# Kernel tuning notes

Hardware: AMD Instinct MI355X
Metric: run time of the kernel (lower is better)

## Reference

```python
import jax, jax.numpy as jnp
import numpy as np
import math

D_MODEL = 256
N_LEVELS = 4
N_HEADS = 8
N_POINTS = 4
N_FRAME = 4
SHAPES = [(80, 80), (40, 40), (20, 20), (10, 10)]  # sum H*W = 8500
NB = 2
T1 = 4
T2 = 4
LEN_Q = 8500


def _grid_init_bias():
    # replicate torch _reset_parameters grid bias for sampling_offsets
    thetas = np.arange(N_HEADS, dtype=np.float32) * (2.0 * math.pi / N_HEADS)
    grid = np.stack([np.cos(thetas), np.sin(thetas)], -1)
    grid = grid / np.abs(grid).max(-1, keepdims=True)
    grid = np.tile(grid[:, None, None, :], (1, N_LEVELS, N_POINTS, 1))
    grid = grid * (np.arange(N_POINTS, dtype=np.float32) + 1.0)[None, None, :, None]
    return jnp.asarray(grid.reshape(-1), jnp.float32)


def setup_inputs() -> dict:
    key = jax.random.key(0)
    ks = jax.random.split(key, 8)
    Len_in = sum(h * w for h, w in SHAPES)
    query = jax.random.normal(ks[0], (NB, T1, LEN_Q, D_MODEL), jnp.float32)
    reference_points = jax.random.uniform(ks[1], (NB, T1, LEN_Q, N_LEVELS, 2), jnp.float32)
    input_flatten = jax.random.normal(ks[2], (NB, T2, Len_in, D_MODEL), jnp.float32)
    input_spatial_shapes = jnp.array(SHAPES, jnp.int32)
    starts = np.cumsum([0] + [h * w for h, w in SHAPES])[:-1]
    input_level_start_index = jnp.asarray(starts, jnp.int32)
    s = 0.01
    W_off = jax.random.normal(ks[3], (D_MODEL, N_HEADS * N_LEVELS * N_POINTS * 2), jnp.float32) * s
    b_off = _grid_init_bias()
    W_att = jax.random.normal(ks[4], (D_MODEL, N_HEADS * N_LEVELS * N_POINTS), jnp.float32) * s
    b_att = jnp.zeros((N_HEADS * N_LEVELS * N_POINTS,), jnp.float32)
    xav = 1.0 / math.sqrt(D_MODEL)
    W_val = jax.random.normal(ks[5], (D_MODEL, D_MODEL), jnp.float32) * xav
    b_val = jnp.zeros((D_MODEL,), jnp.float32)
    W_out = jax.random.normal(ks[6], (D_MODEL, D_MODEL), jnp.float32) * xav
    b_out = jnp.zeros((D_MODEL,), jnp.float32)
    return dict(query=query, reference_points=reference_points, input_flatten=input_flatten,
                input_spatial_shapes=input_spatial_shapes, input_level_start_index=input_level_start_index,
                W_off=W_off, b_off=b_off, W_att=W_att, b_att=b_att,
                W_val=W_val, b_val=b_val, W_out=W_out, b_out=b_out)


def _bilinear(v_flat, H, W, gx, gy):
    # v_flat: (B, d, H*W); gx,gy: (B, S) in [-1,1]; zeros padding, align_corners=False
    x = (gx + 1.0) * (W * 0.5) - 0.5
    y = (gy + 1.0) * (H * 0.5) - 0.5
    x0 = jnp.floor(x); y0 = jnp.floor(y)
    x1 = x0 + 1.0; y1 = y0 + 1.0
    wx1 = x - x0; wx0 = 1.0 - wx1
    wy1 = y - y0; wy0 = 1.0 - wy1

    def gather(xi, yi):
        valid = ((xi >= 0) & (xi < W) & (yi >= 0) & (yi < H)).astype(v_flat.dtype)
        xc = jnp.clip(xi, 0, W - 1).astype(jnp.int32)
        yc = jnp.clip(yi, 0, H - 1).astype(jnp.int32)
        idx = yc * W + xc  # (B, S)
        g = jnp.take_along_axis(v_flat, idx[:, None, :], axis=2)  # (B, d, S)
        return g * valid[:, None, :]

    return (gather(x0, y0) * (wx0 * wy0)[:, None, :]
            + gather(x1, y0) * (wx1 * wy0)[:, None, :]
            + gather(x0, y1) * (wx0 * wy1)[:, None, :]
            + gather(x1, y1) * (wx1 * wy1)[:, None, :])


def _core(value_t, locs, att, shapes):
    # value_t: (n, Len_in, M, d); locs: (n, Lq, M, L, P, 2); att: (n, Lq, M, L, P)
    n, Len_in, M, d = value_t.shape
    Lq, P = locs.shape[1], locs.shape[4]
    start = 0
    out = 0.0
    for l, (H, W) in enumerate(shapes):
        hw = H * W
        v = value_t[:, start:start + hw]  # (n, hw, M, d)
        start += hw
        v = v.transpose(0, 2, 3, 1).reshape(n * M, d, hw)
        g = locs[:, :, :, l] * 2.0 - 1.0  # (n, Lq, M, P, 2)
        g = g.transpose(0, 2, 1, 3, 4).reshape(n * M, Lq * P, 2)
        samp = _bilinear(v, H, W, g[..., 0], g[..., 1])  # (n*M, d, Lq*P)
        a = att[:, :, :, l].transpose(0, 2, 1, 3).reshape(n * M, 1, Lq * P)
        out = out + (samp * a).reshape(n, M, d, Lq, P).sum(-1)
    return out.transpose(0, 3, 1, 2).reshape(n, Lq, M * d)  # (n, Lq, C)


def reference(query, reference_points, input_flatten, input_spatial_shapes, input_level_start_index,
              W_off, b_off, W_att, b_att, W_val, b_val, W_out, b_out):
    shapes = [(int(h), int(w)) for h, w in np.asarray(input_spatial_shapes)]
    n, t1n, Lq, C = query.shape
    M, L, P = N_HEADS, N_LEVELS, N_POINTS
    d = C // M
    value = input_flatten @ W_val + b_val  # (n, T2, Len_in, C)
    value = value.reshape(n, value.shape[1], -1, M, d)
    normalizer = jnp.array([[w, h] for h, w in shapes], jnp.float32)  # (L, 2) = (W_l, H_l)
    outs = []
    for t1 in range(t1n):
        t2s = [t for t in (t1 - 1, t1, t1 + 1) if 0 <= t < N_FRAME]
        K = len(t2s)
        q = query[:, t1]  # (n, Lq, C)
        # all frames share ONE attention_weights Linear -> identical logits per t2
        logits = (q @ W_att + b_att).reshape(n, Lq, M, L, P)
        stacked = jnp.broadcast_to(logits[..., None], (n, Lq, M, L, P, K))
        att = jax.nn.softmax(stacked.reshape(n, Lq, M, L * P * K), axis=-1)
        att = att.reshape(n, Lq, M, L, P, K)
        # all frames share ONE sampling_offsets Linear -> identical locations per t2
        off = (q @ W_off + b_off).reshape(n, Lq, M, L, P, 2)
        off = off / normalizer[None, None, None, :, None, :]
        locs = reference_points[:, t1][:, :, None, :, None, :] + off  # (n,Lq,M,L,P,2)
        out_t1 = 0.0
        for k, t2 in enumerate(t2s):
            out_t1 = out_t1 + _core(value[:, t2], locs, att[..., k], shapes)
        outs.append(out_t1)
    out = jnp.stack(outs, axis=1)  # (n, T1, Lq, C)
    return out @ W_out + b_out
```

## Files before the change

kernel.cpp:

```cpp
#include <hip/hip_runtime.h>

#define LQ 8500

typedef _Float16 half8 __attribute__((ext_vector_type(8)));
typedef float f32x4 __attribute__((ext_vector_type(4)));

__device__ __forceinline__ unsigned short f2h(float f) {
    return __builtin_bit_cast(unsigned short, (_Float16)f);
}
__device__ __forceinline__ float hlo(unsigned w) {
    return (float)__builtin_bit_cast(_Float16, (unsigned short)(w & 0xffffu));
}
__device__ __forceinline__ float hhi(unsigned w) {
    return (float)__builtin_bit_cast(_Float16, (unsigned short)(w >> 16));
}
__device__ __forceinline__ unsigned pk2(float a, float b) {
    return (unsigned)f2h(a) | ((unsigned)f2h(b) << 16);
}

__global__ __launch_bounds__(256) void prep_weights(const float* __restrict__ Woff,
                                                    const float* __restrict__ boff,
                                                    const float* __restrict__ Watt,
                                                    const float* __restrict__ batt,
                                                    const float* __restrict__ Wval,
                                                    const float* __restrict__ Wout,
                                                    unsigned short* __restrict__ Wct,
                                                    unsigned short* __restrict__ Wvt,
                                                    unsigned short* __restrict__ Wot,
                                                    float* __restrict__ bcat) {
    int idx = blockIdx.x * 256 + threadIdx.x;
    if (idx < 98304) {
        int j = idx >> 8, k = idx & 255;
        float v = (j < 256) ? Woff[k * 256 + j] : Watt[k * 128 + (j - 256)];
        Wct[idx] = f2h(v);
    } else if (idx < 98304 + 65536) {
        int t = idx - 98304;
        int n = t >> 8, k = t & 255;
        Wvt[t] = f2h(Wval[k * 256 + n]);
    } else if (idx < 98304 + 131072) {
        int t = idx - 98304 - 65536;
        int n = t >> 8, k = t & 255;
        Wot[t] = f2h(Wout[k * 256 + n]);
    } else if (idx < 98304 + 131072 + 384) {
        int j = idx - 98304 - 131072;
        bcat[j] = (j < 256) ? boff[j] : batt[j - 256];
    }
}

template <int OUTMODE, int ASRC>
__global__ __launch_bounds__(256) void gemm_f16(const void* __restrict__ Avoid,
                                                const unsigned short* __restrict__ Bt,
                                                const float* __restrict__ bias,
                                                void* __restrict__ Cout, int M) {
    __shared__ char lds[32768];
    const int tid = threadIdx.x;
    const int r0 = blockIdx.x * 128, c0 = blockIdx.y * 128;
    const int wid = tid >> 6, lane = tid & 63;
    const int wr = (wid >> 1) * 64, wc = (wid & 1) * 64;

    f32x4 acc[4][4] = {};
    uint4 ra[2], rb[2];

#define LOADT(k0)                                                                      \
    {                                                                                  \
        _Pragma("unroll")                                                              \
        for (int cc = 0; cc < 2; ++cc) {                                               \
            int ch = cc * 256 + tid;                                                   \
            int row = ch >> 2, seg = ch & 3;                                           \
            uint4 va = {0, 0, 0, 0};                                                   \
            int ar = r0 + row;                                                         \
            if (ar < M) {                                                              \
                if (ASRC == 0) {                                                       \
                    va = *reinterpret_cast<const uint4*>(                              \
                        (const unsigned short*)Avoid + (size_t)ar * 256 + (k0) + seg * 8); \
                } else if (ASRC == 1) {                                                \
                    const float4* ap = reinterpret_cast<const float4*>(                \
                        (const float*)Avoid + (size_t)ar * 256 + (k0) + seg * 8);      \
                    float4 a = ap[0], b = ap[1];                                       \
                    va.x = pk2(a.x, a.y); va.y = pk2(a.z, a.w);                        \
                    va.z = pk2(b.x, b.y); va.w = pk2(b.z, b.w);                        \
                } else {                                                               \
                    int g = ar / LQ;                                                   \
                    int pos = ar - g * LQ;                                             \
                    int t1 = g & 3, n = g >> 2;                                        \
                    int t2a = t1 == 0 ? 0 : t1 - 1;                                    \
                    int t2b = t1 == 3 ? 3 : t1 + 1;                                    \
                    float4 s0 = {0, 0, 0, 0}, s1 = {0, 0, 0, 0};                       \
                    for (int t2 = t2a; t2 <= t2b; ++t2) {                              \
                        const float4* p = reinterpret_cast<const float4*>(             \
                            (const float*)Avoid +                                      \
                            ((size_t)(n * 4 + t2) * LQ + pos) * 256 + (k0) + seg * 8); \
                        float4 a = p[0], b = p[1];                                     \
                        s0.x += a.x; s0.y += a.y; s0.z += a.z; s0.w += a.w;            \
                        s1.x += b.x; s1.y += b.y; s1.z += b.z; s1.w += b.w;            \
                    }                                                                  \
                    va.x = pk2(s0.x, s0.y); va.y = pk2(s0.z, s0.w);                    \
                    va.z = pk2(s1.x, s1.y); va.w = pk2(s1.z, s1.w);                    \
                }                                                                      \
            }                                                                          \
            ra[cc] = va;                                                               \
            rb[cc] = *reinterpret_cast<const uint4*>(Bt + (size_t)(c0 + row) * 256 +   \
                                                     (k0) + seg * 8);                  \
        }                                                                              \
    }

#define STORET(b)                                                                      \
    {                                                                                  \
        _Pragma("unroll")                                                              \
        for (int cc = 0; cc < 2; ++cc) {                                               \
            int ch = cc * 256 + tid;                                                   \
            int row = ch >> 2, seg = ch & 3;                                           \
            int byte = (row << 6) + (seg << 4);                                        \
            int swz = byte ^ ((row & 7) << 4);                                         \
            *reinterpret_cast<uint4*>(lds + (b) * 16384 + swz) = ra[cc];               \
            *reinterpret_cast<uint4*>(lds + (b) * 16384 + 8192 + swz) = rb[cc];        \
        }                                                                              \
    }

    LOADT(0);
    STORET(0);
    __syncthreads();

    for (int t = 0; t < 8; ++t) {
        if (t < 7) LOADT((t + 1) * 32);
        char* base = lds + (t & 1) * 16384;
        half8 af[4], bf[4];
#pragma unroll
        for (int i = 0; i < 4; ++i) {
            int rowA = wr + i * 16 + (lane & 15);
            int byteA = (rowA << 6) + ((lane >> 4) << 4);
            af[i] = *reinterpret_cast<const half8*>(base + (byteA ^ ((rowA & 7) << 4)));
            int rowB = wc + i * 16 + (lane & 15);
            int byteB = (rowB << 6) + ((lane >> 4) << 4);
            bf[i] = *reinterpret_cast<const half8*>(base + 8192 + (byteB ^ ((rowB & 7) << 4)));
        }
#pragma unroll
        for (int i = 0; i < 4; ++i)
#pragma unroll
            for (int j = 0; j < 4; ++j)
                acc[i][j] = __builtin_amdgcn_mfma_f32_16x16x32_f16(af[i], bf[j], acc[i][j], 0, 0, 0);
        if (t < 7) STORET((t + 1) & 1);
        __syncthreads();
    }

#pragma unroll
    for (int j = 0; j < 4; ++j) {
        int col = c0 + wc + j * 16 + (lane & 15);
        float bv = bias[col];
#pragma unroll
        for (int i = 0; i < 4; ++i) {
#pragma unroll
            for (int r = 0; r < 4; ++r) {
                int row = r0 + wr + i * 16 + (lane >> 4) * 4 + r;
                if (row >= M) continue;
                float v = acc[i][j][r];
                if (OUTMODE == 1) {
                    int g = row / LQ;
                    int pos = row - g * LQ;
                    int t1 = g & 3;
                    float sc = (t1 == 0 || t1 == 3) ? 2.f : 3.f;
                    v += bv * sc;
                    int m = col >> 5, c = col & 31;
                    ((unsigned short*)Cout)[((size_t)(g * 8 + m) * LQ + pos) * 32 + c] = f2h(v);
                } else if (OUTMODE == 2) {
                    ((unsigned short*)Cout)[(size_t)row * 384 + col] = f2h(v + bv);
                } else {
                    ((float*)Cout)[(size_t)row * 256 + col] = v + bv;
                }
            }
        }
    }
#undef LOADT
#undef STORET
}

__global__ __launch_bounds__(256) void sample_kernel(const unsigned short* __restrict__ P,
                                                     const float* __restrict__ refp,
                                                     const unsigned short* __restrict__ Vs,
                                                     unsigned short* __restrict__ O16) {
    int tid = threadIdx.x, bid = blockIdx.x;
    int g = bid & 7;
    int q0 = (bid >> 3) * 16;
    int ql = tid >> 4, m = (tid >> 1) & 7, h = tid & 1;
    int q = q0 + ql;
    if (q >= LQ) return;

    const size_t qrow = (size_t)g * LQ + q;

    unsigned ow[16];
    {
        const uint4* po = reinterpret_cast<const uint4*>(P + qrow * 384 + m * 32);
        uint4 a = po[0], b = po[1], c = po[2], d = po[3];
        ow[0] = a.x; ow[1] = a.y; ow[2] = a.z; ow[3] = a.w;
        ow[4] = b.x; ow[5] = b.y; ow[6] = b.z; ow[7] = b.w;
        ow[8] = c.x; ow[9] = c.y; ow[10] = c.z; ow[11] = c.w;
        ow[12] = d.x; ow[13] = d.y; ow[14] = d.z; ow[15] = d.w;
    }
    float wgt[16];
    {
        const uint4* pa = reinterpret_cast<const uint4*>(P + qrow * 384 + 256 + m * 16);
        uint4 a = pa[0], b = pa[1];
        unsigned aw[8] = {a.x, a.y, a.z, a.w, b.x, b.y, b.z, b.w};
#pragma unroll
        for (int j = 0; j < 8; ++j) {
            wgt[j * 2 + 0] = hlo(aw[j]);
            wgt[j * 2 + 1] = hhi(aw[j]);
        }
        float mx = -1e30f;
#pragma unroll
        for (int j = 0; j < 16; ++j) mx = fmaxf(mx, wgt[j]);
        float s = 0.f;
#pragma unroll
        for (int j = 0; j < 16; ++j) { wgt[j] = __expf(wgt[j] - mx); s += wgt[j]; }
        int t1 = g & 3;
        float Kc = (t1 == 0 || t1 == 3) ? 2.f : 3.f;
        float inv = 1.f / (s * Kc);
#pragma unroll
        for (int j = 0; j < 16; ++j) wgt[j] *= inv;
    }

    float rx[4], ry[4];
    {
        const float4* rp = reinterpret_cast<const float4*>(refp + qrow * 8);
        float4 r0 = rp[0], r1 = rp[1];
        rx[0] = r0.x; ry[0] = r0.y; rx[1] = r0.z; ry[1] = r0.w;
        rx[2] = r1.x; ry[2] = r1.y; rx[3] = r1.z; ry[3] = r1.w;
    }

    float acc[16];
#pragma unroll
    for (int d = 0; d < 16; ++d) acc[d] = 0.f;

    const unsigned short* vplane = Vs + (size_t)(g * 8 + m) * (LQ * 32) + h * 16;

#pragma unroll 4
    for (int p = 0; p < 16; ++p) {
        const int l = p >> 2;
        const int Wl = 80 >> l;
        const int start = (l == 0) ? 0 : (l == 1) ? 6400 : (l == 2) ? 8000 : 8400;
        const float Wlf = (float)Wl;

        float x = fmaf(rx[l], Wlf, hlo(ow[p])) - 0.5f;
        float y = fmaf(ry[l], Wlf, hhi(ow[p])) - 0.5f;
        float w = wgt[p];

        float xf = floorf(x), yf = floorf(y);
        int x0 = (int)xf, y0 = (int)yf;
        float wx1 = x - xf, wy1 = y - yf;

        int xb = min(max(x0, 0), Wl - 2);
        float wl = (x0 == xb) ? 1.f - wx1 : ((x0 + 1 == xb) ? wx1 : 0.f);
        float wr = (x0 == xb) ? wx1 : ((x0 - 1 == xb) ? 1.f - wx1 : 0.f);

        int yc0 = min(max(y0, 0), Wl - 1);
        float cw0 = (y0 >= 0 && y0 < Wl) ? (1.f - wy1) * w : 0.f;
        int y1i = y0 + 1;
        int yc1 = min(max(y1i, 0), Wl - 1);
        float cw1 = (y1i >= 0 && y1i < Wl) ? wy1 * w : 0.f;

        const uint4* p0 = reinterpret_cast<const uint4*>(
            vplane + (size_t)(start + yc0 * Wl + xb) * 32);
        const uint4* p1 = reinterpret_cast<const uint4*>(
            vplane + (size_t)(start + yc1 * Wl + xb) * 32);
        uint4 L0a = p0[0], L0b = p0[1], R0a = p0[4], R0b = p0[5];
        uint4 L1a = p1[0], L1b = p1[1], R1a = p1[4], R1b = p1[5];

        float c0l = cw0 * wl, c0r = cw0 * wr;
        float c1l = cw1 * wl, c1r = cw1 * wr;

        acc[0]  += c0l * hlo(L0a.x) + c0r * hlo(R0a.x) + c1l * hlo(L1a.x) + c1r * hlo(R1a.x);
        acc[1]  += c0l * hhi(L0a.x) + c0r * hhi(R0a.x) + c1l * hhi(L1a.x) + c1r * hhi(R1a.x);
        acc[2]  += c0l * hlo(L0a.y) + c0r * hlo(R0a.y) + c1l * hlo(L1a.y) + c1r * hlo(R1a.y);
        acc[3]  += c0l * hhi(L0a.y) + c0r * hhi(R0a.y) + c1l * hhi(L1a.y) + c1r * hhi(R1a.y);
        acc[4]  += c0l * hlo(L0a.z) + c0r * hlo(R0a.z) + c1l * hlo(L1a.z) + c1r * hlo(R1a.z);
        acc[5]  += c0l * hhi(L0a.z) + c0r * hhi(R0a.z) + c1l * hhi(L1a.z) + c1r * hhi(R1a.z);
        acc[6]  += c0l * hlo(L0a.w) + c0r * hlo(R0a.w) + c1l * hlo(L1a.w) + c1r * hlo(R1a.w);
        acc[7]  += c0l * hhi(L0a.w) + c0r * hhi(R0a.w) + c1l * hhi(L1a.w) + c1r * hhi(R1a.w);
        acc[8]  += c0l * hlo(L0b.x) + c0r * hlo(R0b.x) + c1l * hlo(L1b.x) + c1r * hlo(R1b.x);
        acc[9]  += c0l * hhi(L0b.x) + c0r * hhi(R0b.x) + c1l * hhi(L1b.x) + c1r * hhi(R1b.x);
        acc[10] += c0l * hlo(L0b.y) + c0r * hlo(R0b.y) + c1l * hlo(L1b.y) + c1r * hlo(R1b.y);
        acc[11] += c0l * hhi(L0b.y) + c0r * hhi(R0b.y) + c1l * hhi(L1b.y) + c1r * hhi(R1b.y);
        acc[12] += c0l * hlo(L0b.z) + c0r * hlo(R0b.z) + c1l * hlo(L1b.z) + c1r * hlo(R1b.z);
        acc[13] += c0l * hhi(L0b.z) + c0r * hhi(R0b.z) + c1l * hhi(L1b.z) + c1r * hhi(R1b.z);
        acc[14] += c0l * hlo(L0b.w) + c0r * hlo(R0b.w) + c1l * hlo(L1b.w) + c1r * hlo(R1b.w);
        acc[15] += c0l * hhi(L0b.w) + c0r * hhi(R0b.w) + c1l * hhi(L1b.w) + c1r * hhi(R1b.w);
    }

    unsigned short* op = O16 + qrow * 256 + m * 32 + h * 16;
    uint4 o0, o1;
    o0.x = pk2(acc[0], acc[1]);   o0.y = pk2(acc[2], acc[3]);
    o0.z = pk2(acc[4], acc[5]);   o0.w = pk2(acc[6], acc[7]);
    o1.x = pk2(acc[8], acc[9]);   o1.y = pk2(acc[10], acc[11]);
    o1.z = pk2(acc[12], acc[13]); o1.w = pk2(acc[14], acc[15]);
    reinterpret_cast<uint4*>(op)[0] = o0;
    reinterpret_cast<uint4*>(op)[1] = o1;
}

extern "C" void kernel_launch(void* const* d_in, const int* in_sizes, int n_in,
                              void* d_out, int out_size, void* d_ws, size_t ws_size,
                              hipStream_t stream) {
    const float* query = (const float*)d_in[0];
    const float* refp  = (const float*)d_in[1];
    const float* inp   = (const float*)d_in[2];
    const float* Woff = (const float*)d_in[5];
    const float* boff = (const float*)d_in[6];
    const float* Watt = (const float*)d_in[7];
    const float* batt = (const float*)d_in[8];
    const float* Wval = (const float*)d_in[9];
    const float* bval = (const float*)d_in[10];
    const float* Wout = (const float*)d_in[11];
    const float* bout = (const float*)d_in[12];
    float* out = (float*)d_out;

    char* base = (char*)d_ws;
    unsigned short* Vs   = (unsigned short*)base;
    unsigned short* P    = (unsigned short*)(base + 34816000);
    unsigned short* O16  = (unsigned short*)(base + 87040000);
    unsigned short* Wct  = (unsigned short*)(base + 121856000);
    unsigned short* Wvt  = (unsigned short*)(base + 122052608);
    unsigned short* Wot  = (unsigned short*)(base + 122183680);
    float* bcat          = (float*)(base + 122314752);

    prep_weights<<<dim3(898), 256, 0, stream>>>(Woff, boff, Watt, batt, Wval, Wout,
                                                Wct, Wvt, Wot, bcat);

    gemm_f16<1, 2><<<dim3((8 * LQ + 127) / 128, 2), 256, 0, stream>>>(
        inp, Wvt, bval, Vs, 8 * LQ);

    gemm_f16<2, 1><<<dim3((8 * LQ + 127) / 128, 3), 256, 0, stream>>>(
        query, Wct, bcat, P, 8 * LQ);

    sample_kernel<<<dim3(((LQ + 15) / 16) * 8), 256, 0, stream>>>(P, refp, Vs, O16);

    gemm_f16<0, 0><<<dim3((8 * LQ + 127) / 128, 2), 256, 0, stream>>>(
        O16, Wot, bout, out, 8 * LQ);
}
```

Measured before the change: 360.8 us.

## Project values before frame summing, cache coarse levels in LDS for sampling

The value projection GEMM now runs on the plain fp32 input and writes an fp16 Y. A new vsum kernel then sums the neighbouring frames and adds the scaled bias into the per-head plane layout. This replaces the three-frame gather that ran inside the GEMM's A-load and cuts redundant fp32 reads. The sample kernel is regridded so each block handles one (g, head) plane for 128 queries, and it preloads the small levels 2 and 3 of that plane into shared memory before sampling them from LDS. The costs are an extra kernel launch, an extra fp16 round trip through the workspace, and summing already-rounded fp16 values.

```diff
diff --git a/kernel.cpp b/kernel.cpp
--- a/kernel.cpp
+++ b/kernel.cpp
@@ -73,29 +73,12 @@
                 if (ASRC == 0) {                                                       \
                     va = *reinterpret_cast<const uint4*>(                              \
                         (const unsigned short*)Avoid + (size_t)ar * 256 + (k0) + seg * 8); \
-                } else if (ASRC == 1) {                                                \
+                } else {                                                               \
                     const float4* ap = reinterpret_cast<const float4*>(                \
                         (const float*)Avoid + (size_t)ar * 256 + (k0) + seg * 8);      \
                     float4 a = ap[0], b = ap[1];                                       \
                     va.x = pk2(a.x, a.y); va.y = pk2(a.z, a.w);                        \
                     va.z = pk2(b.x, b.y); va.w = pk2(b.z, b.w);                        \
-                } else {                                                               \
-                    int g = ar / LQ;                                                   \
-                    int pos = ar - g * LQ;                                             \
-                    int t1 = g & 3, n = g >> 2;                                        \
-                    int t2a = t1 == 0 ? 0 : t1 - 1;                                    \
-                    int t2b = t1 == 3 ? 3 : t1 + 1;                                    \
-                    float4 s0 = {0, 0, 0, 0}, s1 = {0, 0, 0, 0};                       \
-                    for (int t2 = t2a; t2 <= t2b; ++t2) {                              \
-                        const float4* p = reinterpret_cast<const float4*>(             \
-                            (const float*)Avoid +                                      \
-                            ((size_t)(n * 4 + t2) * LQ + pos) * 256 + (k0) + seg * 8); \
-                        float4 a = p[0], b = p[1];                                     \
-                        s0.x += a.x; s0.y += a.y; s0.z += a.z; s0.w += a.w;            \
-                        s1.x += b.x; s1.y += b.y; s1.z += b.z; s1.w += b.w;            \
-                    }                                                                  \
-                    va.x = pk2(s0.x, s0.y); va.y = pk2(s0.z, s0.w);                    \
-                    va.z = pk2(s1.x, s1.y); va.w = pk2(s1.z, s1.w);                    \
                 }                                                                      \
             }                                                                          \
             ra[cc] = va;                                                               \
@@ -146,7 +129,7 @@
 #pragma unroll
     for (int j = 0; j < 4; ++j) {
         int col = c0 + wc + j * 16 + (lane & 15);
-        float bv = bias[col];
+        float bv = (OUTMODE == 3) ? 0.f : bias[col];
 #pragma unroll
         for (int i = 0; i < 4; ++i) {
 #pragma unroll
@@ -154,16 +137,10 @@
                 int row = r0 + wr + i * 16 + (lane >> 4) * 4 + r;
                 if (row >= M) continue;
                 float v = acc[i][j][r];
-                if (OUTMODE == 1) {
-                    int g = row / LQ;
-                    int pos = row - g * LQ;
-                    int t1 = g & 3;
-                    float sc = (t1 == 0 || t1 == 3) ? 2.f : 3.f;
-                    v += bv * sc;
-                    int m = col >> 5, c = col & 31;
-                    ((unsigned short*)Cout)[((size_t)(g * 8 + m) * LQ + pos) * 32 + c] = f2h(v);
-                } else if (OUTMODE == 2) {
+                if (OUTMODE == 2) {
                     ((unsigned short*)Cout)[(size_t)row * 384 + col] = f2h(v + bv);
+                } else if (OUTMODE == 3) {
+                    ((unsigned short*)Cout)[(size_t)row * 256 + col] = f2h(v);
                 } else {
                     ((float*)Cout)[(size_t)row * 256 + col] = v + bv;
                 }
@@ -174,15 +151,58 @@
 #undef STORET
 }
 
+__global__ __launch_bounds__(256) void vsum_kernel(const unsigned short* __restrict__ Y,
+                                                   const float* __restrict__ bval,
+                                                   unsigned short* __restrict__ Vs) {
+    int plane = blockIdx.y;
+    int g = plane >> 3, m = plane & 7;
+    int t1 = g & 3, n = g >> 2;
+    int f = blockIdx.x * 256 + threadIdx.x;
+    if (f >= LQ * 4) return;
+    int pos = f >> 2, c8 = (f & 3) * 8;
+    float Kc = (t1 == 0 || t1 == 3) ? 2.f : 3.f;
+    const float* bp = bval + m * 32 + c8;
+    float acc[8];
+#pragma unroll
+    for (int j = 0; j < 8; ++j) acc[j] = Kc * bp[j];
+    int t2a = t1 == 0 ? 0 : t1 - 1;
+    int t2b = t1 == 3 ? 3 : t1 + 1;
+    for (int t2 = t2a; t2 <= t2b; ++t2) {
+        uint4 v = *reinterpret_cast<const uint4*>(
+            Y + ((size_t)(n * 4 + t2) * LQ + pos) * 256 + m * 32 + c8);
+        acc[0] += hlo(v.x); acc[1] += hhi(v.x);
+        acc[2] += hlo(v.y); acc[3] += hhi(v.y);
+        acc[4] += hlo(v.z); acc[5] += hhi(v.z);
+        acc[6] += hlo(v.w); acc[7] += hhi(v.w);
+    }
+    uint4 o;
+    o.x = pk2(acc[0], acc[1]); o.y = pk2(acc[2], acc[3]);
+    o.z = pk2(acc[4], acc[5]); o.w = pk2(acc[6], acc[7]);
+    *reinterpret_cast<uint4*>(Vs + ((size_t)plane * LQ + pos) * 32 + c8) = o;
+}
+
 __global__ __launch_bounds__(256) void sample_kernel(const unsigned short* __restrict__ P,
                                                      const float* __restrict__ refp,
                                                      const unsigned short* __restrict__ Vs,
                                                      unsigned short* __restrict__ O16) {
+    __shared__ uint4 vlds4[2000];
+
     int tid = threadIdx.x, bid = blockIdx.x;
-    int g = bid & 7;
-    int q0 = (bid >> 3) * 16;
-    int ql = tid >> 4, m = (tid >> 1) & 7, h = tid & 1;
-    int q = q0 + ql;
+    int g = bid & 7, m = (bid >> 3) & 7, qb = bid >> 6;
+    const unsigned short* vplane0 = Vs + (size_t)(g * 8 + m) * (LQ * 32);
+
+    {
+        const uint4* src = reinterpret_cast<const uint4*>(vplane0 + 8000 * 32);
+#pragma unroll
+        for (int i = 0; i < 8; ++i) {
+            int c = i * 256 + tid;
+            if (c < 2000) vlds4[c] = src[c];
+        }
+    }
+    __syncthreads();
+
+    int ql = tid >> 1, h = tid & 1;
+    int q = qb * 128 + ql;
     if (q >= LQ) return;
 
     const size_t qrow = (size_t)g * LQ + q;
@@ -231,60 +251,73 @@
 #pragma unroll
     for (int d = 0; d < 16; ++d) acc[d] = 0.f;
 
-    const unsigned short* vplane = Vs + (size_t)(g * 8 + m) * (LQ * 32) + h * 16;
-
-#pragma unroll 4
-    for (int p = 0; p < 16; ++p) {
+    const unsigned short* vplane = vplane0 + h * 16;
+    const unsigned short* lplane = reinterpret_cast<const unsigned short*>(vlds4) + h * 16;
+
+#define SAMPLE_CORE(Wl, GETP0, GETP1)                                                     \
+    {                                                                                     \
+        float xf = floorf(x), yf = floorf(y);                                             \
+        int x0 = (int)xf, y0 = (int)yf;                                                   \
+        float wx1 = x - xf, wy1 = y - yf;                                                 \
+        int xb = min(max(x0, 0), (Wl)-2);                                                 \
+        float wl = (x0 == xb) ? 1.f - wx1 : ((x0 + 1 == xb) ? wx1 : 0.f);                 \
+        float wr = (x0 == xb) ? wx1 : ((x0 - 1 == xb) ? 1.f - wx1 : 0.f);                 \
+        int yc0 = min(max(y0, 0), (Wl)-1);                                                \
+        float cw0 = (y0 >= 0 && y0 < (Wl)) ? (1.f - wy1) * w : 0.f;                       \
+        int y1i = y0 + 1;                                                                 \
+        int yc1 = min(max(y1i, 0), (Wl)-1);                                               \
+        float cw1 = (y1i >= 0 && y1i < (Wl)) ? wy1 * w : 0.f;                             \
+        const uint4* p0 = (GETP0);                                                        \
+        const uint4* p1 = (GETP1);                                                        \
+        uint4 L0a = p0[0], L0b = p0[1], R0a = p0[4], R0b = p0[5];                         \
+        uint4 L1a = p1[0], L1b = p1[1], R1a = p1[4], R1b = p1[5];                         \
+        float c0l = cw0 * wl, c0r = cw0 * wr;                                             \
+        float c1l = cw1 * wl, c1r = cw1 * wr;                                             \
+        acc[0]  += c0l * hlo(L0a.x) + c0r * hlo(R0a.x) + c1l * hlo(L1a.x) + c1r * hlo(R1a.x); \
+        acc[1]  += c0l * hhi(L0a.x) + c0r * hhi(R0a.x) + c1l * hhi(L1a.x) + c1r * hhi(R1a.x); \
+        acc[2]  += c0l * hlo(L0a.y) + c0r * hlo(R0a.y) + c1l * hlo(L1a.y) + c1r * hlo(R1a.y); \
+        acc[3]  += c0l * hhi(L0a.y) + c0r * hhi(R0a.y) + c1l * hhi(L1a.y) + c1r * hhi(R1a.y); \
+        acc[4]  += c0l * hlo(L0a.z) + c0r * hlo(R0a.z) + c1l * hlo(L1a.z) + c1r * hlo(R1a.z); \
+        acc[5]  += c0l * hhi(L0a.z) + c0r * hhi(R0a.z) + c1l * hhi(L1a.z) + c1r * hhi(R1a.z); \
+        acc[6]  += c0l * hlo(L0a.w) + c0r * hlo(R0a.w) + c1l * hlo(L1a.w) + c1r * hlo(R1a.w); \
+        acc[7]  += c0l * hhi(L0a.w) + c0r * hhi(R0a.w) + c1l * hhi(L1a.w) + c1r * hhi(R1a.w); \
+        acc[8]  += c0l * hlo(L0b.x) + c0r * hlo(R0b.x) + c1l * hlo(L1b.x) + c1r * hlo(R1b.x); \
+        acc[9]  += c0l * hhi(L0b.x) + c0r * hhi(R0b.x) + c1l * hhi(L1b.x) + c1r * hhi(R1b.x); \
+        acc[10] += c0l * hlo(L0b.y) + c0r * hlo(R0b.y) + c1l * hlo(L1b.y) + c1r * hlo(R1b.y); \
+        acc[11] += c0l * hhi(L0b.y) + c0r * hhi(R0b.y) + c1l * hhi(L1b.y) + c1r * hhi(R1b.y); \
+        acc[12] += c0l * hlo(L0b.z) + c0r * hlo(R0b.z) + c1l * hlo(L1b.z) + c1r * hlo(R1b.z); \
+        acc[13] += c0l * hhi(L0b.z) + c0r * hhi(R0b.z) + c1l * hhi(L1b.z) + c1r * hhi(R1b.z); \
+        acc[14] += c0l * hlo(L0b.w) + c0r * hlo(R0b.w) + c1l * hlo(L1b.w) + c1r * hlo(R1b.w); \
+        acc[15] += c0l * hhi(L0b.w) + c0r * hhi(R0b.w) + c1l * hhi(L1b.w) + c1r * hhi(R1b.w); \
+    }
+
+#pragma unroll
+    for (int p = 0; p < 8; ++p) {
         const int l = p >> 2;
         const int Wl = 80 >> l;
-        const int start = (l == 0) ? 0 : (l == 1) ? 6400 : (l == 2) ? 8000 : 8400;
+        const int start = (l == 0) ? 0 : 6400;
         const float Wlf = (float)Wl;
-
         float x = fmaf(rx[l], Wlf, hlo(ow[p])) - 0.5f;
         float y = fmaf(ry[l], Wlf, hhi(ow[p])) - 0.5f;
         float w = wgt[p];
-
-        float xf = floorf(x), yf = floorf(y);
-        int x0 = (int)xf, y0 = (int)yf;
-        float wx1 = x - xf, wy1 = y - yf;
-
-        int xb = min(max(x0, 0), Wl - 2);
-        float wl = (x0 == xb) ? 1.f - wx1 : ((x0 + 1 == xb) ? wx1 : 0.f);
-        float wr = (x0 == xb) ? wx1 : ((x0 - 1 == xb) ? 1.f - wx1 : 0.f);
-
-        int yc0 = min(max(y0, 0), Wl - 1);
-        float cw0 = (y0 >= 0 && y0 < Wl) ? (1.f - wy1) * w : 0.f;
-        int y1i = y0 + 1;
-        int yc1 = min(max(y1i, 0), Wl - 1);
-        float cw1 = (y1i >= 0 && y1i < Wl) ? wy1 * w : 0.f;
-
-        const uint4* p0 = reinterpret_cast<const uint4*>(
-            vplane + (size_t)(start + yc0 * Wl + xb) * 32);
-        const uint4* p1 = reinterpret_cast<const uint4*>(
-            vplane + (size_t)(start + yc1 * Wl + xb) * 32);
-        uint4 L0a = p0[0], L0b = p0[1], R0a = p0[4], R0b = p0[5];
-        uint4 L1a = p1[0], L1b = p1[1], R1a = p1[4], R1b = p1[5];
-
-        float c0l = cw0 * wl, c0r = cw0 * wr;
-        float c1l = cw1 * wl, c1r = cw1 * wr;
-
-        acc[0]  += c0l * hlo(L0a.x) + c0r * hlo(R0a.x) + c1l * hlo(L1a.x) + c1r * hlo(R1a.x);
-        acc[1]  += c0l * hhi(L0a.x) + c0r * hhi(R0a.x) + c1l * hhi(L1a.x) + c1r * hhi(R1a.x);
-        acc[2]  += c0l * hlo(L0a.y) + c0r * hlo(R0a.y) + c1l * hlo(L1a.y) + c1r * hlo(R1a.y);
-        acc[3]  += c0l * hhi(L0a.y) + c0r * hhi(R0a.y) + c1l * hhi(L1a.y) + c1r * hhi(R1a.y);
-        acc[4]  += c0l * hlo(L0a.z) + c0r * hlo(R0a.z) + c1l * hlo(L1a.z) + c1r * hlo(R1a.z);
-        acc[5]  += c0l * hhi(L0a.z) + c0r * hhi(R0a.z) + c1l * hhi(L1a.z) + c1r * hhi(R1a.z);
-        acc[6]  += c0l * hlo(L0a.w) + c0r * hlo(R0a.w) + c1l * hlo(L1a.w) + c1r * hlo(R1a.w);
-        acc[7]  += c0l * hhi(L0a.w) + c0r * hhi(R0a.w) + c1l * hhi(L1a.w) + c1r * hhi(R1a.w);
-        acc[8]  += c0l * hlo(L0b.x) + c0r * hlo(R0b.x) + c1l * hlo(L1b.x) + c1r * hlo(R1b.x);
-        acc[9]  += c0l * hhi(L0b.x) + c0r * hhi(R0b.x) + c1l * hhi(L1b.x) + c1r * hhi(R1b.x);
-        acc[10] += c0l * hlo(L0b.y) + c0r * hlo(R0b.y) + c1l * hlo(L1b.y) + c1r * hlo(R1b.y);
-        acc[11] += c0l * hhi(L0b.y) + c0r * hhi(R0b.y) + c1l * hhi(L1b.y) + c1r * hhi(R1b.y);
-        acc[12] += c0l * hlo(L0b.z) + c0r * hlo(R0b.z) + c1l * hlo(L1b.z) + c1r * hlo(R1b.z);
-        acc[13] += c0l * hhi(L0b.z) + c0r * hhi(R0b.z) + c1l * hhi(L1b.z) + c1r * hhi(R1b.z);
-        acc[14] += c0l * hlo(L0b.w) + c0r * hlo(R0b.w) + c1l * hlo(L1b.w) + c1r * hlo(R1b.w);
-        acc[15] += c0l * hhi(L0b.w) + c0r * hhi(R0b.w) + c1l * hhi(L1b.w) + c1r * hhi(R1b.w);
-    }
+        SAMPLE_CORE(Wl,
+            reinterpret_cast<const uint4*>(vplane + (size_t)(start + yc0 * Wl + xb) * 32),
+            reinterpret_cast<const uint4*>(vplane + (size_t)(start + yc1 * Wl + xb) * 32));
+    }
+#pragma unroll
+    for (int p = 8; p < 16; ++p) {
+        const int l = p >> 2;
+        const int Wl = 80 >> l;
+        const int lbase = (l == 2) ? 0 : 400;
+        const float Wlf = (float)Wl;
+        float x = fmaf(rx[l], Wlf, hlo(ow[p])) - 0.5f;
+        float y = fmaf(ry[l], Wlf, hhi(ow[p])) - 0.5f;
+        float w = wgt[p];
+        SAMPLE_CORE(Wl,
+            reinterpret_cast<const uint4*>(lplane + (lbase + yc0 * Wl + xb) * 32),
+            reinterpret_cast<const uint4*>(lplane + (lbase + yc1 * Wl + xb) * 32));
+    }
+#undef SAMPLE_CORE
 
     unsigned short* op = O16 + qrow * 256 + m * 32 + h * 16;
     uint4 o0, o1;
@@ -313,25 +346,27 @@
     float* out = (float*)d_out;
 
     char* base = (char*)d_ws;
-    unsigned short* Vs   = (unsigned short*)base;
-    unsigned short* P    = (unsigned short*)(base + 34816000);
-    unsigned short* O16  = (unsigned short*)(base + 87040000);
+    unsigned short* Y    = (unsigned short*)base;
+    unsigned short* O16  = (unsigned short*)base;
+    unsigned short* Vs   = (unsigned short*)(base + 34816000);
+    unsigned short* P    = (unsigned short*)(base + 69632000);
     unsigned short* Wct  = (unsigned short*)(base + 121856000);
     unsigned short* Wvt  = (unsigned short*)(base + 122052608);
     unsigned short* Wot  = (unsigned short*)(base + 122183680);
     float* bcat          = (float*)(base + 122314752);
 
+    const int RT = (8 * LQ + 127) / 128;
+
     prep_weights<<<dim3(898), 256, 0, stream>>>(Woff, boff, Watt, batt, Wval, Wout,
                                                 Wct, Wvt, Wot, bcat);
 
-    gemm_f16<1, 2><<<dim3((8 * LQ + 127) / 128, 2), 256, 0, stream>>>(
-        inp, Wvt, bval, Vs, 8 * LQ);
-
-    gemm_f16<2, 1><<<dim3((8 * LQ + 127) / 128, 3), 256, 0, stream>>>(
-        query, Wct, bcat, P, 8 * LQ);
-
-    sample_kernel<<<dim3(((LQ + 15) / 16) * 8), 256, 0, stream>>>(P, refp, Vs, O16);
-
-    gemm_f16<0, 0><<<dim3((8 * LQ + 127) / 128, 2), 256, 0, stream>>>(
-        O16, Wot, bout, out, 8 * LQ);
-}
+    gemm_f16<3, 1><<<dim3(RT, 2), 256, 0, stream>>>(inp, Wvt, bcat, Y, 8 * LQ);
+
+    vsum_kernel<<<dim3((LQ * 4 + 255) / 256, 64), 256, 0, stream>>>(Y, bval, Vs);
+
+    gemm_f16<2, 1><<<dim3(RT, 3), 256, 0, stream>>>(query, Wct, bcat, P, 8 * LQ);
+
+    sample_kernel<<<dim3(((LQ + 127) / 128) * 64), 256, 0, stream>>>(P, refp, Vs, O16);
+
+    gemm_f16<0, 0><<<dim3(RT, 2), 256, 0, stream>>>(O16, Wot, bout, out, 8 * LQ);
+}
```

Result: slower. 389.8 us (+8.0%).

## Project values once then sum neighbor frames in separate kernel; split sampling threads

Applied to the files above, without the earlier changes.

The value GEMM previously read and summed up to three fp32 input frames per row before projecting. Now it projects each frame's input once into an fp16 buffer, and a new vsum kernel adds the neighbouring frames' projected values plus the scaled bias into the head-planar layout. This cuts the GEMM's input reads by up to 3x in exchange for an extra fp16 pass through memory. The sampling kernel is also reorganised: two threads now share each (query, head, half) and each handles half of the sampling points. A shuffle combines their partial sums, which doubles thread-level parallelism for the gather.

```diff
diff --git a/kernel.cpp b/kernel.cpp
--- a/kernel.cpp
+++ b/kernel.cpp
@@ -73,29 +73,12 @@
                 if (ASRC == 0) {                                                       \
                     va = *reinterpret_cast<const uint4*>(                              \
                         (const unsigned short*)Avoid + (size_t)ar * 256 + (k0) + seg * 8); \
-                } else if (ASRC == 1) {                                                \
+                } else {                                                               \
                     const float4* ap = reinterpret_cast<const float4*>(                \
                         (const float*)Avoid + (size_t)ar * 256 + (k0) + seg * 8);      \
                     float4 a = ap[0], b = ap[1];                                       \
                     va.x = pk2(a.x, a.y); va.y = pk2(a.z, a.w);                        \
                     va.z = pk2(b.x, b.y); va.w = pk2(b.z, b.w);                        \
-                } else {                                                               \
-                    int g = ar / LQ;                                                   \
-                    int pos = ar - g * LQ;                                             \
-                    int t1 = g & 3, n = g >> 2;                                        \
-                    int t2a = t1 == 0 ? 0 : t1 - 1;                                    \
-                    int t2b = t1 == 3 ? 3 : t1 + 1;                                    \
-                    float4 s0 = {0, 0, 0, 0}, s1 = {0, 0, 0, 0};                       \
-                    for (int t2 = t2a; t2 <= t2b; ++t2) {                              \
-                        const float4* p = reinterpret_cast<const float4*>(             \
-                            (const float*)Avoid +                                      \
-                            ((size_t)(n * 4 + t2) * LQ + pos) * 256 + (k0) + seg * 8); \
-                        float4 a = p[0], b = p[1];                                     \
-                        s0.x += a.x; s0.y += a.y; s0.z += a.z; s0.w += a.w;            \
-                        s1.x += b.x; s1.y += b.y; s1.z += b.z; s1.w += b.w;            \
-                    }                                                                  \
-                    va.x = pk2(s0.x, s0.y); va.y = pk2(s0.z, s0.w);                    \
-                    va.z = pk2(s1.x, s1.y); va.w = pk2(s1.z, s1.w);                    \
                 }                                                                      \
             }                                                                          \
             ra[cc] = va;                                                               \
@@ -146,7 +129,7 @@
 #pragma unroll
     for (int j = 0; j < 4; ++j) {
         int col = c0 + wc + j * 16 + (lane & 15);
-        float bv = bias[col];
+        float bv = (OUTMODE == 3) ? 0.f : bias[col];
 #pragma unroll
         for (int i = 0; i < 4; ++i) {
 #pragma unroll
@@ -154,16 +137,10 @@
                 int row = r0 + wr + i * 16 + (lane >> 4) * 4 + r;
                 if (row >= M) continue;
                 float v = acc[i][j][r];
-                if (OUTMODE == 1) {
-                    int g = row / LQ;
-                    int pos = row - g * LQ;
-                    int t1 = g & 3;
-                    float sc = (t1 == 0 || t1 == 3) ? 2.f : 3.f;
-                    v += bv * sc;
-                    int m = col >> 5, c = col & 31;
-                    ((unsigned short*)Cout)[((size_t)(g * 8 + m) * LQ + pos) * 32 + c] = f2h(v);
-                } else if (OUTMODE == 2) {
+                if (OUTMODE == 2) {
                     ((unsigned short*)Cout)[(size_t)row * 384 + col] = f2h(v + bv);
+                } else if (OUTMODE == 3) {
+                    ((unsigned short*)Cout)[(size_t)row * 256 + col] = f2h(v);
                 } else {
                     ((float*)Cout)[(size_t)row * 256 + col] = v + bv;
                 }
@@ -172,6 +149,36 @@
     }
 #undef LOADT
 #undef STORET
+}
+
+__global__ __launch_bounds__(256) void vsum_kernel(const unsigned short* __restrict__ Y,
+                                                   const float* __restrict__ bval,
+                                                   unsigned short* __restrict__ Vs) {
+    int plane = blockIdx.y;
+    int g = plane >> 3, m = plane & 7;
+    int t1 = g & 3, n = g >> 2;
+    int f = blockIdx.x * 256 + threadIdx.x;
+    if (f >= LQ * 4) return;
+    int pos = f >> 2, c8 = (f & 3) * 8;
+    float Kc = (t1 == 0 || t1 == 3) ? 2.f : 3.f;
+    const float* bp = bval + m * 32 + c8;
+    float acc[8];
+#pragma unroll
+    for (int j = 0; j < 8; ++j) acc[j] = Kc * bp[j];
+    int t2a = t1 == 0 ? 0 : t1 - 1;
+    int t2b = t1 == 3 ? 3 : t1 + 1;
+    for (int t2 = t2a; t2 <= t2b; ++t2) {
+        uint4 v = *reinterpret_cast<const uint4*>(
+            Y + ((size_t)(n * 4 + t2) * LQ + pos) * 256 + m * 32 + c8);
+        acc[0] += hlo(v.x); acc[1] += hhi(v.x);
+        acc[2] += hlo(v.y); acc[3] += hhi(v.y);
+        acc[4] += hlo(v.z); acc[5] += hhi(v.z);
+        acc[6] += hlo(v.w); acc[7] += hhi(v.w);
+    }
+    uint4 o;
+    o.x = pk2(acc[0], acc[1]); o.y = pk2(acc[2], acc[3]);
+    o.z = pk2(acc[4], acc[5]); o.w = pk2(acc[6], acc[7]);
+    *reinterpret_cast<uint4*>(Vs + ((size_t)plane * LQ + pos) * 32 + c8) = o;
 }
 
 __global__ __launch_bounds__(256) void sample_kernel(const unsigned short* __restrict__ P,
@@ -180,8 +187,11 @@
                                                      unsigned short* __restrict__ O16) {
     int tid = threadIdx.x, bid = blockIdx.x;
     int g = bid & 7;
-    int q0 = (bid >> 3) * 16;
-    int ql = tid >> 4, m = (tid >> 1) & 7, h = tid & 1;
+    int q0 = (bid >> 3) * 8;
+    int ql = tid >> 5;
+    int m = (tid >> 2) & 7;
+    int h = (tid >> 1) & 1;
+    int s = tid & 1;
     int q = q0 + ql;
     if (q >= LQ) return;
 
@@ -196,11 +206,16 @@
         ow[8] = c.x; ow[9] = c.y; ow[10] = c.z; ow[11] = c.w;
         ow[12] = d.x; ow[13] = d.y; ow[14] = d.z; ow[15] = d.w;
     }
-    float wgt[16];
+    unsigned ows[8];
+#pragma unroll
+    for (int j = 0; j < 8; ++j) ows[j] = s ? ow[2 * j + 1] : ow[2 * j];
+
+    float w8[8];
     {
         const uint4* pa = reinterpret_cast<const uint4*>(P + qrow * 384 + 256 + m * 16);
         uint4 a = pa[0], b = pa[1];
         unsigned aw[8] = {a.x, a.y, a.z, a.w, b.x, b.y, b.z, b.w};
+        float wgt[16];
 #pragma unroll
         for (int j = 0; j < 8; ++j) {
             wgt[j * 2 + 0] = hlo(aw[j]);
@@ -209,14 +224,15 @@
         float mx = -1e30f;
 #pragma unroll
         for (int j = 0; j < 16; ++j) mx = fmaxf(mx, wgt[j]);
-        float s = 0.f;
-#pragma unroll
-        for (int j = 0; j < 16; ++j) { wgt[j] = __expf(wgt[j] - mx); s += wgt[j]; }
+        float ssum = 0.f;
+#pragma unroll
+        for (int j = 0; j < 16; ++j) { wgt[j] = __expf(wgt[j] - mx); ssum += wgt[j]; }
         int t1 = g & 3;
         float Kc = (t1 == 0 || t1 == 3) ? 2.f : 3.f;
-        float inv = 1.f / (s * Kc);
-#pragma unroll
-        for (int j = 0; j < 16; ++j) wgt[j] *= inv;
+        float inv = 1.f / (ssum * Kc);
+#pragma unroll
+        for (int j = 0; j < 8; ++j)
+            w8[j] = (s ? wgt[2 * j + 1] : wgt[2 * j]) * inv;
     }
 
     float rx[4], ry[4];
@@ -233,16 +249,16 @@
 
     const unsigned short* vplane = Vs + (size_t)(g * 8 + m) * (LQ * 32) + h * 16;
 
-#pragma unroll 4
-    for (int p = 0; p < 16; ++p) {
-        const int l = p >> 2;
+#pragma unroll
+    for (int j = 0; j < 8; ++j) {
+        const int l = j >> 1;
         const int Wl = 80 >> l;
         const int start = (l == 0) ? 0 : (l == 1) ? 6400 : (l == 2) ? 8000 : 8400;
         const float Wlf = (float)Wl;
 
-        float x = fmaf(rx[l], Wlf, hlo(ow[p])) - 0.5f;
-        float y = fmaf(ry[l], Wlf, hhi(ow[p])) - 0.5f;
-        float w = wgt[p];
+        float x = fmaf(rx[l], Wlf, hlo(ows[j])) - 0.5f;
+        float y = fmaf(ry[l], Wlf, hhi(ows[j])) - 0.5f;
+        float w = w8[j];
 
         float xf = floorf(x), yf = floorf(y);
         int x0 = (int)xf, y0 = (int)yf;
@@ -286,14 +302,18 @@
         acc[15] += c0l * hhi(L0b.w) + c0r * hhi(R0b.w) + c1l * hhi(L1b.w) + c1r * hhi(R1b.w);
     }
 
-    unsigned short* op = O16 + qrow * 256 + m * 32 + h * 16;
-    uint4 o0, o1;
-    o0.x = pk2(acc[0], acc[1]);   o0.y = pk2(acc[2], acc[3]);
-    o0.z = pk2(acc[4], acc[5]);   o0.w = pk2(acc[6], acc[7]);
-    o1.x = pk2(acc[8], acc[9]);   o1.y = pk2(acc[10], acc[11]);
-    o1.z = pk2(acc[12], acc[13]); o1.w = pk2(acc[14], acc[15]);
-    reinterpret_cast<uint4*>(op)[0] = o0;
-    reinterpret_cast<uint4*>(op)[1] = o1;
+#pragma unroll
+    for (int d = 0; d < 16; ++d) acc[d] += __shfl_xor(acc[d], 1);
+
+    float o8[8];
+#pragma unroll
+    for (int j = 0; j < 8; ++j) o8[j] = s ? acc[8 + j] : acc[j];
+
+    unsigned short* op = O16 + qrow * 256 + m * 32 + h * 16 + s * 8;
+    uint4 o;
+    o.x = pk2(o8[0], o8[1]); o.y = pk2(o8[2], o8[3]);
+    o.z = pk2(o8[4], o8[5]); o.w = pk2(o8[6], o8[7]);
+    *reinterpret_cast<uint4*>(op) = o;
 }
 
 extern "C" void kernel_launch(void* const* d_in, const int* in_sizes, int n_in,
@@ -313,25 +333,27 @@
     float* out = (float*)d_out;
 
     char* base = (char*)d_ws;
-    unsigned short* Vs   = (unsigned short*)base;
-    unsigned short* P    = (unsigned short*)(base + 34816000);
-    unsigned short* O16  = (unsigned short*)(base + 87040000);
+    unsigned short* Y    = (unsigned short*)base;
+    unsigned short* O16  = (unsigned short*)base;
+    unsigned short* Vs   = (unsigned short*)(base + 34816000);
+    unsigned short* P    = (unsigned short*)(base + 69632000);
     unsigned short* Wct  = (unsigned short*)(base + 121856000);
     unsigned short* Wvt  = (unsigned short*)(base + 122052608);
     unsigned short* Wot  = (unsigned short*)(base + 122183680);
     float* bcat          = (float*)(base + 122314752);
 
+    const int RT = (8 * LQ + 127) / 128;
+
     prep_weights<<<dim3(898), 256, 0, stream>>>(Woff, boff, Watt, batt, Wval, Wout,
                                                 Wct, Wvt, Wot, bcat);
 
-    gemm_f16<1, 2><<<dim3((8 * LQ + 127) / 128, 2), 256, 0, stream>>>(
-        inp, Wvt, bval, Vs, 8 * LQ);
-
-    gemm_f16<2, 1><<<dim3((8 * LQ + 127) / 128, 3), 256, 0, stream>>>(
-        query, Wct, bcat, P, 8 * LQ);
-
-    sample_kernel<<<dim3(((LQ + 15) / 16) * 8), 256, 0, stream>>>(P, refp, Vs, O16);
-
-    gemm_f16<0, 0><<<dim3((8 * LQ + 127) / 128, 2), 256, 0, stream>>>(
-        O16, Wot, bout, out, 8 * LQ);
-}
+    gemm_f16<3, 1><<<dim3(RT, 2), 256, 0, stream>>>(inp, Wvt, bcat, Y, 8 * LQ);
+
+    vsum_kernel<<<dim3((LQ * 4 + 255) / 256, 64), 256, 0, stream>>>(Y, bval, Vs);
+
+    gemm_f16<2, 1><<<dim3(RT, 3), 256, 0, stream>>>(query, Wct, bcat, P, 8 * LQ);
+
+    sample_kernel<<<dim3(((LQ + 7) / 8) * 8), 256, 0, stream>>>(P, refp, Vs, O16);
+
+    gemm_f16<0, 0><<<dim3(RT, 2), 256, 0, stream>>>(O16, Wot, bout, out, 8 * LQ);
+}
```

Measured after the change: 616.5 us. 70.9% more time.
